# Performance work log

Hardware: AMD Instinct MI355X
Metric: run time of the kernel (lower is better)

The kernel has to match this reference:

```python
import jax, jax.numpy as jnp
import numpy as np

DIM = 256
HEADS = 8
WIN = 8
HIDDEN = 1024
EPS = 1e-5

def _rel_pos_index(w):
    coords = np.stack(np.meshgrid(np.arange(w), np.arange(w), indexing='ij'))  # [2,w,w]
    cf = coords.reshape(2, -1)
    rel = cf[:, :, None] - cf[:, None, :]  # [2,N,N]
    rel = rel.transpose(1, 2, 0)
    rel[:, :, 0] += w - 1
    rel[:, :, 1] += w - 1
    rel[:, :, 0] *= 2 * w - 1
    return jnp.asarray(rel.sum(-1))  # [N,N] int

REL_IDX = _rel_pos_index(WIN)

def _layernorm(x, g, b):
    mu = jnp.mean(x, -1, keepdims=True)
    var = jnp.mean(jnp.square(x - mu), -1, keepdims=True)
    return (x - mu) * jax.lax.rsqrt(var + EPS) * g + b

def setup_inputs() -> dict:
    key = jax.random.key(0)
    ks = jax.random.split(key, 12)
    s = 0.02
    return {
        'x': jax.random.normal(ks[0], (16, 4096, 256), jnp.float32),
        'H': 64,
        'W': 64,
        'ln1_g': jnp.ones((DIM,), jnp.float32),
        'ln1_b': jnp.zeros((DIM,), jnp.float32),
        'qkv_w': jax.random.normal(ks[1], (DIM, 3 * DIM), jnp.float32) * s,
        'proj_w': jax.random.normal(ks[2], (DIM, DIM), jnp.float32) * s,
        'proj_b': jnp.zeros((DIM,), jnp.float32),
        'rel_bias_table': jax.random.normal(ks[3], ((2 * WIN - 1) ** 2, HEADS), jnp.float32) * s,
        'ln2_g': jnp.ones((DIM,), jnp.float32),
        'ln2_b': jnp.zeros((DIM,), jnp.float32),
        'fc1_w': jax.random.normal(ks[4], (DIM, HIDDEN), jnp.float32) * s,
        'fc1_b': jnp.zeros((HIDDEN,), jnp.float32),
        'fc2_w': jax.random.normal(ks[5], (HIDDEN, DIM), jnp.float32) * s,
        'fc2_b': jnp.zeros((DIM,), jnp.float32),
    }

def reference(x, H, W, ln1_g, ln1_b, qkv_w, proj_w, proj_b, rel_bias_table,
              ln2_g, ln2_b, fc1_w, fc1_b, fc2_w, fc2_b):
    B, L, C = x.shape
    w = WIN
    N = w * w
    head_dim = C // HEADS
    scale = head_dim ** -0.5

    shortcut = x
    h = _layernorm(x, ln1_g, ln1_b).reshape(B, H, W, C)
    # H, W chosen divisible by window_size -> pad_h = pad_w = 0 (faithful fast path)
    # window partition: [B*nW, N, C]
    h = h.reshape(B, H // w, w, W // w, w, C).transpose(0, 1, 3, 2, 4, 5)
    xw = h.reshape(-1, N, C)
    Bw = xw.shape[0]

    qkv = (xw @ qkv_w).reshape(Bw, N, 3, HEADS, head_dim)
    q = qkv[:, :, 0].transpose(0, 2, 1, 3) * scale  # [Bw,h,N,d]
    k = qkv[:, :, 1].transpose(0, 2, 1, 3)
    v = qkv[:, :, 2].transpose(0, 2, 1, 3)

    attn = jnp.einsum('bhnd,bhmd->bhnm', q, k)
    bias = rel_bias_table[REL_IDX.reshape(-1)].reshape(N, N, HEADS).transpose(2, 0, 1)
    attn = jax.nn.softmax(attn + bias[None], axis=-1)
    out = jnp.einsum('bhnm,bhmd->bhnd', attn, v).transpose(0, 2, 1, 3).reshape(Bw, N, C)
    out = out @ proj_w + proj_b

    # window reverse
    out = out.reshape(B, H // w, W // w, w, w, C).transpose(0, 1, 3, 2, 4, 5)
    out = out.reshape(B, L, C)

    x = shortcut + out
    h2 = _layernorm(x, ln2_g, ln2_b)
    mlp = jax.nn.gelu(h2 @ fc1_w + fc1_b, approximate=False) @ fc2_w + fc2_b
    return x + mlp
```

## Files before the change

kernel.cpp:

```cpp
#include <hip/hip_runtime.h>
#include <hip/hip_bf16.h>

typedef __attribute__((ext_vector_type(8))) short bf16x8;
typedef __attribute__((ext_vector_type(4))) float f32x4;

typedef __attribute__((address_space(3))) void LdsVoid;
typedef const __attribute__((address_space(1))) void GblVoid;

__device__ __forceinline__ void gload16(const void* g, void* l) {
  __builtin_amdgcn_global_load_lds((GblVoid*)g, (LdsVoid*)l, 16, 0, 0);
}

__device__ __forceinline__ unsigned short f2bf(float f) {
  union { float f; unsigned int u; } x; x.f = f;
  unsigned int r = (x.u + 0x7fffu + ((x.u >> 16) & 1u)) >> 16;
  return (unsigned short)r;
}

__device__ __forceinline__ float gelu_f(float t) {
  float u = t * (0.7978845608028654f + 0.03567740814f * t * t);
  float e = __expf(2.0f * u);
  float th = 1.0f - 2.0f * __builtin_amdgcn_rcpf(e + 1.0f);
  return 0.5f * t * (1.0f + th);
}

__global__ __launch_bounds__(256) void prep_w(
    const float* __restrict__ qw, const float* __restrict__ pw,
    const float* __restrict__ f1, const float* __restrict__ f2,
    unsigned short* __restrict__ out) {
  int idx = blockIdx.x * 256 + threadIdx.x;
  if (idx < 196608) { int n = idx >> 8, k = idx & 255; out[idx] = f2bf(qw[k * 768 + n]); return; }
  int i2 = idx - 196608;
  if (i2 < 65536) { int n = i2 >> 8, k = i2 & 255; out[idx] = f2bf(pw[k * 256 + n]); return; }
  int i3 = i2 - 65536;
  if (i3 < 262144) { int n = i3 >> 8, k = i3 & 255; out[idx] = f2bf(f1[k * 1024 + n]); return; }
  int i4 = i3 - 262144;
  { int n = i4 >> 10, k = i4 & 1023; out[idx] = f2bf(f2[k * 256 + n]); }
}

__global__ __launch_bounds__(256) void ln1_kernel(
    const float* __restrict__ x, const float* __restrict__ g, const float* __restrict__ b,
    unsigned short* __restrict__ xn) {
  int lane = threadIdx.x & 63, wid = threadIdx.x >> 6;
  size_t t = (size_t)blockIdx.x * 4 + wid;
  float4 v = ((const float4*)(x + t * 256))[lane];
  float s = v.x + v.y + v.z + v.w;
  #pragma unroll
  for (int m = 1; m < 64; m <<= 1) s += __shfl_xor(s, m);
  float mean = s * (1.0f / 256.0f);
  float dx = v.x - mean, dy = v.y - mean, dz = v.z - mean, dw = v.w - mean;
  float q = dx * dx + dy * dy + dz * dz + dw * dw;
  #pragma unroll
  for (int m = 1; m < 64; m <<= 1) q += __shfl_xor(q, m);
  float rstd = rsqrtf(q * (1.0f / 256.0f) + 1e-5f);
  float4 gg = ((const float4*)g)[lane];
  float4 bb = ((const float4*)b)[lane];
  unsigned int o0 = f2bf(dx * rstd * gg.x + bb.x) | ((unsigned int)f2bf(dy * rstd * gg.y + bb.y) << 16);
  unsigned int o1 = f2bf(dz * rstd * gg.z + bb.z) | ((unsigned int)f2bf(dw * rstd * gg.w + bb.w) << 16);
  int bI = (int)(t >> 12), rem = (int)t & 4095, y = rem >> 6, xc = rem & 63;
  size_t r = ((size_t)(bI * 64 + (y >> 3) * 8 + (xc >> 3))) * 64 + (y & 7) * 8 + (xc & 7);
  uint2 o; o.x = o0; o.y = o1;
  ((uint2*)(xn + r * 256))[lane] = o;
}

template <int EPI>
__global__ __launch_bounds__(256) void gemm_bt(
    const unsigned short* __restrict__ A, const unsigned short* __restrict__ Bt,
    unsigned short* __restrict__ outb, float* __restrict__ outf,
    const float* __restrict__ bias, const float* __restrict__ xres,
    int M, int N, int K) {
  __shared__ __align__(16) unsigned short lds[2 * 8192];
  const int tid = threadIdx.x;
  const int lane = tid & 63, wid = tid >> 6;
  const int cl = lane & 15, cg = lane >> 4;
  const unsigned nwg = gridDim.x * gridDim.y;
  const unsigned orig = blockIdx.y * gridDim.x + blockIdx.x;
  const unsigned virt = (orig & 7) * (nwg >> 3) + (orig >> 3);
  const unsigned bx = virt % gridDim.x, by = virt / gridDim.x;
  const size_t m0 = (size_t)by * 128;
  const size_t n0 = (size_t)bx * 128;
  const int wr = wid >> 1, wc = wid & 1;
  f32x4 acc[4][4] = {};

  const int r4 = lane >> 2;
  const int gsw = ((lane & 3) ^ ((r4 >> 1) & 3)) * 8;
  const unsigned short* aStage = A + (m0 + wid * 32 + r4) * K + gsw;
  const unsigned short* bStage = Bt + (n0 + wid * 32 + r4) * K + gsw;
  const size_t jstep = (size_t)16 * K;
  const int nt = K >> 5;

  #define STAGE(T, B)                                                   \
    { const int ko_ = (T) * 32;                                         \
      unsigned short* la_ = lds + (B) * 8192 + wid * 1024;              \
      unsigned short* lb_ = la_ + 4096;                                 \
      gload16(aStage + ko_, la_);                                       \
      gload16(aStage + ko_ + jstep, la_ + 512);                         \
      gload16(bStage + ko_, lb_);                                       \
      gload16(bStage + ko_ + jstep, lb_ + 512); }

  bf16x8 af[4], bfr[4];
  const int sl_ = (cg ^ ((cl >> 1) & 3)) * 8;
  #define READF(B)                                                          \
    { const unsigned short* base_ = lds + (B) * 8192;                       \
      _Pragma("unroll")                                                     \
      for (int i = 0; i < 4; ++i) {                                         \
        af[i]  = *(const bf16x8*)(base_ + (wr * 64 + i * 16 + cl) * 32 + sl_);        \
        bfr[i] = *(const bf16x8*)(base_ + 4096 + (wc * 64 + i * 16 + cl) * 32 + sl_); \
      } }

  #define MFMAS()                                                           \
    { _Pragma("unroll")                                                     \
      for (int mi = 0; mi < 4; ++mi)                                        \
        _Pragma("unroll")                                                   \
        for (int ni = 0; ni < 4; ++ni)                                      \
          acc[mi][ni] = __builtin_amdgcn_mfma_f32_16x16x32_bf16(bfr[ni], af[mi], acc[mi][ni], 0, 0, 0); }

  STAGE(0, 0);
  STAGE(1, 1);
  for (int t = 0; t < nt; ++t) {
    if (t == nt - 1) { asm volatile("s_waitcnt vmcnt(0)" ::: "memory"); }
    else             { asm volatile("s_waitcnt vmcnt(4)" ::: "memory"); }
    __builtin_amdgcn_s_barrier();
    READF(t & 1);
    __builtin_amdgcn_sched_barrier(0);
    asm volatile("s_waitcnt lgkmcnt(0)" ::: "memory");
    __builtin_amdgcn_s_barrier();
    __builtin_amdgcn_sched_barrier(0);
    if (t + 2 < nt) STAGE(t + 2, t & 1);
    MFMAS();
  }
  #undef STAGE
  #undef READF
  #undef MFMAS

  #pragma unroll
  for (int mi = 0; mi < 4; ++mi) {
    const size_t row = m0 + wr * 64 + mi * 16 + cl;
    #pragma unroll
    for (int ni = 0; ni < 4; ++ni) {
      const size_t col = n0 + wc * 64 + ni * 16 + cg * 4;
      f32x4 v = acc[mi][ni];
      if (EPI == 0) {
        uint2 o;
        o.x = f2bf(v[0]) | ((unsigned int)f2bf(v[1]) << 16);
        o.y = f2bf(v[2]) | ((unsigned int)f2bf(v[3]) << 16);
        *(uint2*)&outb[row * N + col] = o;
      } else if (EPI == 1) {
        float4 bb = *(const float4*)&bias[col];
        float g0 = gelu_f(v[0] + bb.x), g1 = gelu_f(v[1] + bb.y);
        float g2 = gelu_f(v[2] + bb.z), g3 = gelu_f(v[3] + bb.w);
        uint2 o;
        o.x = f2bf(g0) | ((unsigned int)f2bf(g1) << 16);
        o.y = f2bf(g2) | ((unsigned int)f2bf(g3) << 16);
        *(uint2*)&outb[row * N + col] = o;
      } else if (EPI == 3) {
        float4 bb = *(const float4*)&bias[col];
        float4* p = (float4*)&outf[row * N + col];
        float4 old = *p;
        old.x += v[0] + bb.x; old.y += v[1] + bb.y;
        old.z += v[2] + bb.z; old.w += v[3] + bb.w;
        *p = old;
      } else if (EPI == 4) {
        int winr = (int)(row >> 6), pos = (int)(row & 63);
        int bI = winr >> 6, wy = (winr >> 3) & 7, wx = winr & 7;
        size_t tt = (size_t)bI * 4096 + (size_t)(wy * 8 + (pos >> 3)) * 64 + wx * 8 + (pos & 7);
        float4 bb = *(const float4*)&bias[col];
        float4 xr = *(const float4*)&xres[tt * 256 + col];
        float4 o;
        o.x = v[0] + bb.x + xr.x; o.y = v[1] + bb.y + xr.y;
        o.z = v[2] + bb.z + xr.z; o.w = v[3] + bb.w + xr.w;
        *(float4*)&outf[tt * 256 + col] = o;
      }
    }
  }
}

__global__ __launch_bounds__(256) void attn_win(
    const unsigned short* __restrict__ qkv, const float* __restrict__ table,
    unsigned short* __restrict__ out) {
  __shared__ float tbl[1800];
  __shared__ __align__(16) unsigned short p_lds[4][64 * 72];
  __shared__ __align__(16) unsigned short vt_lds[4][32 * 72];
  const int tid = threadIdx.x, lane = tid & 63, wid = tid >> 6;
  const int cl = lane & 15, cg = lane >> 4;
  for (int i = tid; i < 1800; i += 256) tbl[i] = table[i];
  __syncthreads();
  const size_t wbase = (size_t)blockIdx.x * 64;
  unsigned short* P = p_lds[wid];
  unsigned short* VT = vt_lds[wid];
  const float scale = 0.17677669529663687f;

  for (int hh = 0; hh < 2; ++hh) {
    const int h = wid + hh * 4;
    const int qoff = h * 32, koff = 256 + h * 32, voff = 512 + h * 32;
    bf16x8 qf[4], kf[4];
    #pragma unroll
    for (int mi = 0; mi < 4; ++mi)
      qf[mi] = *(const bf16x8*)&qkv[(wbase + mi * 16 + cl) * 768 + qoff + cg * 8];
    #pragma unroll
    for (int nj = 0; nj < 4; ++nj)
      kf[nj] = *(const bf16x8*)&qkv[(wbase + nj * 16 + cl) * 768 + koff + cg * 8];
    f32x4 S[4][4] = {};
    #pragma unroll
    for (int mi = 0; mi < 4; ++mi)
      #pragma unroll
      for (int nj = 0; nj < 4; ++nj)
        S[mi][nj] = __builtin_amdgcn_mfma_f32_16x16x32_bf16(qf[mi], kf[nj], S[mi][nj], 0, 0, 0);

    {
      const unsigned short* vrow = &qkv[(wbase + lane) * 768 + voff];
      unsigned short tmp[32];
      #pragma unroll
      for (int p = 0; p < 4; ++p) *(uint4*)&tmp[p * 8] = ((const uint4*)vrow)[p];
      #pragma unroll
      for (int d = 0; d < 32; ++d) VT[d * 72 + lane] = tmp[d];
    }

    #pragma unroll
    for (int mi = 0; mi < 4; ++mi) {
      #pragma unroll
      for (int r = 0; r < 4; ++r) {
        const int i = mi * 16 + cg * 4 + r;
        const int yi = i >> 3, xi = i & 7;
        float v[4];
        float m = -1e30f;
        #pragma unroll
        for (int nj = 0; nj < 4; ++nj) {
          const int j = nj * 16 + cl;
          const int yj = j >> 3, xj = j & 7;
          float bia = tbl[((yi - yj + 7) * 15 + (xi - xj + 7)) * 8 + h];
          v[nj] = S[mi][nj][r] * scale + bia;
          m = fmaxf(m, v[nj]);
        }
        #pragma unroll
        for (int mk = 1; mk < 16; mk <<= 1) m = fmaxf(m, __shfl_xor(m, mk));
        float s = 0.0f;
        #pragma unroll
        for (int nj = 0; nj < 4; ++nj) { v[nj] = __expf(v[nj] - m); s += v[nj]; }
        #pragma unroll
        for (int mk = 1; mk < 16; mk <<= 1) s += __shfl_xor(s, mk);
        const float rinv = __builtin_amdgcn_rcpf(s);
        #pragma unroll
        for (int nj = 0; nj < 4; ++nj) P[i * 72 + nj * 16 + cl] = f2bf(v[nj] * rinv);
      }
    }

    f32x4 O[4][2] = {};
    #pragma unroll
    for (int ks = 0; ks < 2; ++ks) {
      bf16x8 pa[4], vb[2];
      #pragma unroll
      for (int mi = 0; mi < 4; ++mi)
        pa[mi] = *(const bf16x8*)&P[(mi * 16 + cl) * 72 + ks * 32 + cg * 8];
      #pragma unroll
      for (int nd = 0; nd < 2; ++nd)
        vb[nd] = *(const bf16x8*)&VT[(nd * 16 + cl) * 72 + ks * 32 + cg * 8];
      #pragma unroll
      for (int mi = 0; mi < 4; ++mi)
        #pragma unroll
        for (int nd = 0; nd < 2; ++nd)
          O[mi][nd] = __builtin_amdgcn_mfma_f32_16x16x32_bf16(vb[nd], pa[mi], O[mi][nd], 0, 0, 0);
    }

    #pragma unroll
    for (int mi = 0; mi < 4; ++mi)
      #pragma unroll
      for (int nd = 0; nd < 2; ++nd) {
        uint2 o;
        o.x = f2bf(O[mi][nd][0]) | ((unsigned int)f2bf(O[mi][nd][1]) << 16);
        o.y = f2bf(O[mi][nd][2]) | ((unsigned int)f2bf(O[mi][nd][3]) << 16);
        *(uint2*)&out[(wbase + mi * 16 + cl) * 256 + h * 32 + nd * 16 + cg * 4] = o;
      }
  }
}

__global__ __launch_bounds__(256) void ln2_kernel(
    const float* __restrict__ x2, const float* __restrict__ g, const float* __restrict__ b,
    unsigned short* __restrict__ h2) {
  int lane = threadIdx.x & 63, wid = threadIdx.x >> 6;
  size_t t = (size_t)blockIdx.x * 4 + wid;
  float4 v = ((const float4*)(x2 + t * 256))[lane];
  float s = v.x + v.y + v.z + v.w;
  #pragma unroll
  for (int m = 1; m < 64; m <<= 1) s += __shfl_xor(s, m);
  float mean = s * (1.0f / 256.0f);
  float dx = v.x - mean, dy = v.y - mean, dz = v.z - mean, dw = v.w - mean;
  float q = dx * dx + dy * dy + dz * dz + dw * dw;
  #pragma unroll
  for (int m = 1; m < 64; m <<= 1) q += __shfl_xor(q, m);
  float rstd = rsqrtf(q * (1.0f / 256.0f) + 1e-5f);
  float4 gg = ((const float4*)g)[lane];
  float4 bb = ((const float4*)b)[lane];
  uint2 o;
  o.x = f2bf(dx * rstd * gg.x + bb.x) | ((unsigned int)f2bf(dy * rstd * gg.y + bb.y) << 16);
  o.y = f2bf(dz * rstd * gg.z + bb.z) | ((unsigned int)f2bf(dw * rstd * gg.w + bb.w) << 16);
  ((uint2*)(h2 + t * 256))[lane] = o;
}

extern "C" void kernel_launch(void* const* d_in, const int* in_sizes, int n_in,
                              void* d_out, int out_size, void* d_ws, size_t ws_size,
                              hipStream_t stream) {
  (void)in_sizes; (void)n_in; (void)out_size; (void)ws_size;
  const float* x       = (const float*)d_in[0];
  const float* ln1_g   = (const float*)d_in[3];
  const float* ln1_b   = (const float*)d_in[4];
  const float* qkv_w   = (const float*)d_in[5];
  const float* proj_w  = (const float*)d_in[6];
  const float* proj_b  = (const float*)d_in[7];
  const float* rel_tbl = (const float*)d_in[8];
  const float* ln2_g   = (const float*)d_in[9];
  const float* ln2_b   = (const float*)d_in[10];
  const float* fc1_w   = (const float*)d_in[11];
  const float* fc1_b   = (const float*)d_in[12];
  const float* fc2_w   = (const float*)d_in[13];
  const float* fc2_b   = (const float*)d_in[14];
  float* out = (float*)d_out;

  char* ws = (char*)d_ws;
  const size_t OFF_XN   = 1572864;
  const size_t OFF_QKV  = OFF_XN + 33554432;
  const size_t OFF_ATTN = OFF_QKV + 100663296;
  unsigned short* Wt      = (unsigned short*)ws;
  unsigned short* xn      = (unsigned short*)(ws + OFF_XN);
  unsigned short* h2      = xn;
  unsigned short* qkv     = (unsigned short*)(ws + OFF_QKV);
  unsigned short* fc1out  = (unsigned short*)(ws + OFF_QKV);
  unsigned short* attnout = (unsigned short*)(ws + OFF_ATTN);

  prep_w<<<3072, 256, 0, stream>>>(qkv_w, proj_w, fc1_w, fc2_w, Wt);
  ln1_kernel<<<16384, 256, 0, stream>>>(x, ln1_g, ln1_b, xn);
  gemm_bt<0><<<dim3(6, 512), 256, 0, stream>>>(xn, Wt, qkv, nullptr, nullptr, nullptr, 65536, 768, 256);
  attn_win<<<1024, 256, 0, stream>>>(qkv, rel_tbl, attnout);
  gemm_bt<4><<<dim3(2, 512), 256, 0, stream>>>(attnout, Wt + 196608, nullptr, out, proj_b, x, 65536, 256, 256);
  ln2_kernel<<<16384, 256, 0, stream>>>(out, ln2_g, ln2_b, h2);
  gemm_bt<1><<<dim3(8, 512), 256, 0, stream>>>(h2, Wt + 262144, fc1out, nullptr, fc1_b, nullptr, 65536, 1024, 256);
  gemm_bt<3><<<dim3(2, 512), 256, 0, stream>>>(fc1out, Wt + 524288, nullptr, out, fc2_b, nullptr, 65536, 256, 1024);
}
```

Before: 430.6 us.

## Replace 128x128 GEMM with 256x256 8-wave ping-pong pipelined GEMM

Replaces the 4-wave 128x128-tile GEMM with an 8-wave kernel that computes 256x256 tiles using a 64-wide K step, 128 KB of dynamic LDS, and a four-phase loop. Each phase issues LDS reads and global-to-LDS loads for quarter-tiles and runs MFMA under raised priority. The goal is more operand reuse per loaded byte and better overlap of memory traffic with MFMA work. The larger tile halves or thirds the grid sizes, which lowers parallelism across the 65536-row GEMMs. With 128 KB of LDS per block, occupancy is probably about one block per CU, which may not match launch_bounds(512,2), and the extra barriers add synchronisation cost.

```diff
diff --git a/kernel.cpp b/kernel.cpp
--- a/kernel.cpp
+++ b/kernel.cpp
@@ -64,82 +64,113 @@
 }
 
 template <int EPI>
-__global__ __launch_bounds__(256) void gemm_bt(
+__global__ __launch_bounds__(512, 2) void gemm8p(
     const unsigned short* __restrict__ A, const unsigned short* __restrict__ Bt,
     unsigned short* __restrict__ outb, float* __restrict__ outf,
     const float* __restrict__ bias, const float* __restrict__ xres,
     int M, int N, int K) {
-  __shared__ __align__(16) unsigned short lds[2 * 8192];
+  extern __shared__ unsigned short lds[];
   const int tid = threadIdx.x;
-  const int lane = tid & 63, wid = tid >> 6;
+  const int lane = tid & 63, w = tid >> 6;
   const int cl = lane & 15, cg = lane >> 4;
+  const int wr = w >> 2, wc = w & 3;
   const unsigned nwg = gridDim.x * gridDim.y;
   const unsigned orig = blockIdx.y * gridDim.x + blockIdx.x;
   const unsigned virt = (orig & 7) * (nwg >> 3) + (orig >> 3);
   const unsigned bx = virt % gridDim.x, by = virt / gridDim.x;
-  const size_t m0 = (size_t)by * 128;
-  const size_t n0 = (size_t)bx * 128;
-  const int wr = wid >> 1, wc = wid & 1;
-  f32x4 acc[4][4] = {};
-
-  const int r4 = lane >> 2;
-  const int gsw = ((lane & 3) ^ ((r4 >> 1) & 3)) * 8;
-  const unsigned short* aStage = A + (m0 + wid * 32 + r4) * K + gsw;
-  const unsigned short* bStage = Bt + (n0 + wid * 32 + r4) * K + gsw;
-  const size_t jstep = (size_t)16 * K;
-  const int nt = K >> 5;
-
-  #define STAGE(T, B)                                                   \
-    { const int ko_ = (T) * 32;                                         \
-      unsigned short* la_ = lds + (B) * 8192 + wid * 1024;              \
-      unsigned short* lb_ = la_ + 4096;                                 \
-      gload16(aStage + ko_, la_);                                       \
-      gload16(aStage + ko_ + jstep, la_ + 512);                         \
-      gload16(bStage + ko_, lb_);                                       \
-      gload16(bStage + ko_ + jstep, lb_ + 512); }
-
-  bf16x8 af[4], bfr[4];
-  const int sl_ = (cg ^ ((cl >> 1) & 3)) * 8;
-  #define READF(B)                                                          \
-    { const unsigned short* base_ = lds + (B) * 8192;                       \
-      _Pragma("unroll")                                                     \
-      for (int i = 0; i < 4; ++i) {                                         \
-        af[i]  = *(const bf16x8*)(base_ + (wr * 64 + i * 16 + cl) * 32 + sl_);        \
-        bfr[i] = *(const bf16x8*)(base_ + 4096 + (wc * 64 + i * 16 + cl) * 32 + sl_); \
-      } }
-
-  #define MFMAS()                                                           \
-    { _Pragma("unroll")                                                     \
-      for (int mi = 0; mi < 4; ++mi)                                        \
-        _Pragma("unroll")                                                   \
-        for (int ni = 0; ni < 4; ++ni)                                      \
-          acc[mi][ni] = __builtin_amdgcn_mfma_f32_16x16x32_bf16(bfr[ni], af[mi], acc[mi][ni], 0, 0, 0); }
-
-  STAGE(0, 0);
-  STAGE(1, 1);
-  for (int t = 0; t < nt; ++t) {
-    if (t == nt - 1) { asm volatile("s_waitcnt vmcnt(0)" ::: "memory"); }
-    else             { asm volatile("s_waitcnt vmcnt(4)" ::: "memory"); }
-    __builtin_amdgcn_s_barrier();
-    READF(t & 1);
-    __builtin_amdgcn_sched_barrier(0);
-    asm volatile("s_waitcnt lgkmcnt(0)" ::: "memory");
-    __builtin_amdgcn_s_barrier();
-    __builtin_amdgcn_sched_barrier(0);
-    if (t + 2 < nt) STAGE(t + 2, t & 1);
-    MFMAS();
+  const size_t m0 = (size_t)by * 256, n0 = (size_t)bx * 256;
+  const int nkt = K >> 6;
+
+  const int trow = tid >> 3, tslot = tid & 7;
+  const unsigned short* aSrc = A + (m0 + trow) * K + (tslot ^ (trow & 7)) * 8;
+  const unsigned short* bSrc = Bt + (n0 + trow) * K + (tslot ^ (trow & 7)) * 8;
+
+  const int slk0 = ((0 + cg) ^ (cl & 7)) * 8;
+  const int slk1 = ((4 + cg) ^ (cl & 7)) * 8;
+
+  f32x4 acc[8][4] = {};
+  bf16x8 af[2][4], b0[2][2], b1[2][2];
+
+  #define STAGE(ISB, KT, HALF)                                                    \
+    { unsigned short* d_ = lds + (ISB) * 32768 + ((KT) & 1) * 16384 +             \
+                           (HALF) * 8192 + tid * 8;                               \
+      const unsigned short* s_ = ((ISB) ? bSrc : aSrc) +                          \
+                                 (size_t)((HALF) * 128) * K + (KT) * 64;          \
+      gload16(s_, d_); gload16(s_ + (size_t)64 * K, d_ + 4096); }
+
+  #define READ_A(MH, P)                                                           \
+    { const unsigned short* ba_ = lds + (P) * 16384 + (MH) * 8192 +               \
+                                  (wr * 64 + cl) * 64;                            \
+      _Pragma("unroll")                                                           \
+      for (int mi = 0; mi < 4; ++mi) {                                            \
+        af[0][mi] = *(const bf16x8*)(ba_ + mi * 1024 + slk0);                     \
+        af[1][mi] = *(const bf16x8*)(ba_ + mi * 1024 + slk1); } }
+
+  #define READ_B(NH, P, D)                                                        \
+    { const unsigned short* bb_ = lds + 32768 + (P) * 16384 + (NH) * 8192 +       \
+                                  (wc * 32 + cl) * 64;                            \
+      _Pragma("unroll")                                                           \
+      for (int ni = 0; ni < 2; ++ni) {                                            \
+        D[0][ni] = *(const bf16x8*)(bb_ + ni * 1024 + slk0);                      \
+        D[1][ni] = *(const bf16x8*)(bb_ + ni * 1024 + slk1); } }
+
+  #define MFMA_Q(MH, NH, D)                                                       \
+    { _Pragma("unroll")                                                           \
+      for (int kk = 0; kk < 2; ++kk)                                              \
+        _Pragma("unroll")                                                         \
+        for (int mi = 0; mi < 4; ++mi)                                            \
+          _Pragma("unroll")                                                       \
+          for (int ni = 0; ni < 2; ++ni)                                          \
+            acc[(MH) * 4 + mi][(NH) * 2 + ni] =                                   \
+                __builtin_amdgcn_mfma_f32_16x16x32_bf16(                          \
+                    D[kk][ni], af[kk][mi], acc[(MH) * 4 + mi][(NH) * 2 + ni],     \
+                    0, 0, 0); }
+
+  #define BAR() __builtin_amdgcn_s_barrier()
+  #define LGKM0() { asm volatile("s_waitcnt lgkmcnt(0)" ::: "memory");            \
+                    __builtin_amdgcn_sched_barrier(0); }
+
+  STAGE(0, 0, 0); STAGE(1, 0, 1); STAGE(1, 0, 0); STAGE(0, 0, 1);
+  STAGE(0, 1, 0); STAGE(1, 1, 1);
+  asm volatile("s_waitcnt vmcnt(4)" ::: "memory");
+  BAR();
+
+  for (int kt = 0; kt < nkt; ++kt) {
+    const int p = kt & 1;
+    READ_A(0, p); READ_B(0, p, b0);
+    if (kt + 1 < nkt) STAGE(1, kt + 1, 0);
+    BAR(); LGKM0();
+    __builtin_amdgcn_s_setprio(1); MFMA_Q(0, 0, b0); __builtin_amdgcn_s_setprio(0);
+    BAR();
+    READ_B(1, p, b1);
+    if (kt + 1 < nkt) STAGE(0, kt + 1, 1);
+    BAR(); LGKM0();
+    __builtin_amdgcn_s_setprio(1); MFMA_Q(0, 1, b1); __builtin_amdgcn_s_setprio(0);
+    BAR();
+    READ_A(1, p);
+    if (kt + 2 < nkt) STAGE(0, kt + 2, 0);
+    BAR(); LGKM0();
+    __builtin_amdgcn_s_setprio(1); MFMA_Q(1, 1, b1); __builtin_amdgcn_s_setprio(0);
+    BAR();
+    if (kt + 2 < nkt) STAGE(1, kt + 2, 1);
+    BAR();
+    __builtin_amdgcn_s_setprio(1); MFMA_Q(1, 0, b0); __builtin_amdgcn_s_setprio(0);
+    if (kt + 2 < nkt) { asm volatile("s_waitcnt vmcnt(4)" ::: "memory"); }
+    else              { asm volatile("s_waitcnt vmcnt(0)" ::: "memory"); }
+    BAR();
   }
   #undef STAGE
-  #undef READF
-  #undef MFMAS
-
-  #pragma unroll
-  for (int mi = 0; mi < 4; ++mi) {
-    const size_t row = m0 + wr * 64 + mi * 16 + cl;
-    #pragma unroll
-    for (int ni = 0; ni < 4; ++ni) {
-      const size_t col = n0 + wc * 64 + ni * 16 + cg * 4;
-      f32x4 v = acc[mi][ni];
+  #undef READ_A
+  #undef READ_B
+  #undef MFMA_Q
+
+  #pragma unroll
+  for (int mi8 = 0; mi8 < 8; ++mi8) {
+    const size_t row = m0 + (mi8 >> 2) * 128 + wr * 64 + (mi8 & 3) * 16 + cl;
+    #pragma unroll
+    for (int ni4 = 0; ni4 < 4; ++ni4) {
+      const size_t col = n0 + (ni4 >> 1) * 128 + wc * 32 + (ni4 & 1) * 16 + cg * 4;
+      f32x4 v = acc[mi8][ni4];
       if (EPI == 0) {
         uint2 o;
         o.x = f2bf(v[0]) | ((unsigned int)f2bf(v[1]) << 16);
@@ -155,11 +186,11 @@
         *(uint2*)&outb[row * N + col] = o;
       } else if (EPI == 3) {
         float4 bb = *(const float4*)&bias[col];
-        float4* p = (float4*)&outf[row * N + col];
-        float4 old = *p;
+        float4* pp = (float4*)&outf[row * N + col];
+        float4 old = *pp;
         old.x += v[0] + bb.x; old.y += v[1] + bb.y;
         old.z += v[2] + bb.z; old.w += v[3] + bb.w;
-        *p = old;
+        *pp = old;
       } else if (EPI == 4) {
         int winr = (int)(row >> 6), pos = (int)(row & 63);
         int bI = winr >> 6, wy = (winr >> 3) & 7, wx = winr & 7;
@@ -327,12 +358,19 @@
   unsigned short* fc1out  = (unsigned short*)(ws + OFF_QKV);
   unsigned short* attnout = (unsigned short*)(ws + OFF_ATTN);
 
+  static int attr_done = -1;
+  if (attr_done < 0) attr_done = 0;
+  hipFuncSetAttribute((const void*)gemm8p<0>, hipFuncAttributeMaxDynamicSharedMemorySize, 131072);
+  hipFuncSetAttribute((const void*)gemm8p<1>, hipFuncAttributeMaxDynamicSharedMemorySize, 131072);
+  hipFuncSetAttribute((const void*)gemm8p<3>, hipFuncAttributeMaxDynamicSharedMemorySize, 131072);
+  hipFuncSetAttribute((const void*)gemm8p<4>, hipFuncAttributeMaxDynamicSharedMemorySize, 131072);
+
   prep_w<<<3072, 256, 0, stream>>>(qkv_w, proj_w, fc1_w, fc2_w, Wt);
   ln1_kernel<<<16384, 256, 0, stream>>>(x, ln1_g, ln1_b, xn);
-  gemm_bt<0><<<dim3(6, 512), 256, 0, stream>>>(xn, Wt, qkv, nullptr, nullptr, nullptr, 65536, 768, 256);
+  gemm8p<0><<<dim3(3, 256), 512, 131072, stream>>>(xn, Wt, qkv, nullptr, nullptr, nullptr, 65536, 768, 256);
   attn_win<<<1024, 256, 0, stream>>>(qkv, rel_tbl, attnout);
-  gemm_bt<4><<<dim3(2, 512), 256, 0, stream>>>(attnout, Wt + 196608, nullptr, out, proj_b, x, 65536, 256, 256);
+  gemm8p<4><<<dim3(1, 256), 512, 131072, stream>>>(attnout, Wt + 196608, nullptr, out, proj_b, x, 65536, 256, 256);
   ln2_kernel<<<16384, 256, 0, stream>>>(out, ln2_g, ln2_b, h2);
-  gemm_bt<1><<<dim3(8, 512), 256, 0, stream>>>(h2, Wt + 262144, fc1out, nullptr, fc1_b, nullptr, 65536, 1024, 256);
-  gemm_bt<3><<<dim3(2, 512), 256, 0, stream>>>(fc1out, Wt + 524288, nullptr, out, fc2_b, nullptr, 65536, 256, 1024);
-}
+  gemm8p<1><<<dim3(4, 256), 512, 131072, stream>>>(h2, Wt + 262144, fc1out, nullptr, fc1_b, nullptr, 65536, 1024, 256);
+  gemm8p<3><<<dim3(1, 256), 512, 131072, stream>>>(fc1out, Wt + 524288, nullptr, out, fc2_b, nullptr, 65536, 256, 1024);
+}
```

Result: no change. 424.3 us (-1.4%).

## Replace LDS-staged GEMM with register-resident weight tiles and direct A loads

Applied to the files above, without the earlier changes.

The shared-memory double-buffered GEMM is replaced by a kernel that keeps a 64-column slice of the weight matrix, for a full 256-wide K chunk, in registers. Each wave streams its A rows straight from global memory with one-step register prefetch and covers 128 rows in two 64-row tiles. This removes LDS staging, barriers and waitcnt handling, and reuses the loaded weights across both row tiles when K fits in one chunk. The costs are high register pressure (32 bf16x8 weight fragments per lane), uncoalesced 16-byte A loads with no cross-wave sharing, and each A row being reloaded once per 64-column block, which can make the kernel bandwidth-bound.

```diff
diff --git a/kernel.cpp b/kernel.cpp
--- a/kernel.cpp
+++ b/kernel.cpp
@@ -3,13 +3,6 @@
 
 typedef __attribute__((ext_vector_type(8))) short bf16x8;
 typedef __attribute__((ext_vector_type(4))) float f32x4;
-
-typedef __attribute__((address_space(3))) void LdsVoid;
-typedef const __attribute__((address_space(1))) void GblVoid;
-
-__device__ __forceinline__ void gload16(const void* g, void* l) {
-  __builtin_amdgcn_global_load_lds((GblVoid*)g, (LdsVoid*)l, 16, 0, 0);
-}
 
 __device__ __forceinline__ unsigned short f2bf(float f) {
   union { float f; unsigned int u; } x; x.f = f;
@@ -63,113 +56,97 @@
   ((uint2*)(xn + r * 256))[lane] = o;
 }
 
-template <int EPI>
-__global__ __launch_bounds__(256) void gemm_bt(
+template <int EPI, int KC>
+__global__ __launch_bounds__(256, 2) void gemm_flat(
     const unsigned short* __restrict__ A, const unsigned short* __restrict__ Bt,
     unsigned short* __restrict__ outb, float* __restrict__ outf,
     const float* __restrict__ bias, const float* __restrict__ xres,
-    int M, int N, int K) {
-  __shared__ __align__(16) unsigned short lds[2 * 8192];
-  const int tid = threadIdx.x;
-  const int lane = tid & 63, wid = tid >> 6;
+    int N, int K) {
+  const int tid = threadIdx.x, lane = tid & 63, w = tid >> 6;
   const int cl = lane & 15, cg = lane >> 4;
-  const unsigned nwg = gridDim.x * gridDim.y;
-  const unsigned orig = blockIdx.y * gridDim.x + blockIdx.x;
-  const unsigned virt = (orig & 7) * (nwg >> 3) + (orig >> 3);
-  const unsigned bx = virt % gridDim.x, by = virt / gridDim.x;
-  const size_t m0 = (size_t)by * 128;
-  const size_t n0 = (size_t)bx * 128;
-  const int wr = wid >> 1, wc = wid & 1;
-  f32x4 acc[4][4] = {};
-
-  const int r4 = lane >> 2;
-  const int gsw = ((lane & 3) ^ ((r4 >> 1) & 3)) * 8;
-  const unsigned short* aStage = A + (m0 + wid * 32 + r4) * K + gsw;
-  const unsigned short* bStage = Bt + (n0 + wid * 32 + r4) * K + gsw;
-  const size_t jstep = (size_t)16 * K;
-  const int nt = K >> 5;
-
-  #define STAGE(T, B)                                                   \
-    { const int ko_ = (T) * 32;                                         \
-      unsigned short* la_ = lds + (B) * 8192 + wid * 1024;              \
-      unsigned short* lb_ = la_ + 4096;                                 \
-      gload16(aStage + ko_, la_);                                       \
-      gload16(aStage + ko_ + jstep, la_ + 512);                         \
-      gload16(bStage + ko_, lb_);                                       \
-      gload16(bStage + ko_ + jstep, lb_ + 512); }
-
-  bf16x8 af[4], bfr[4];
-  const int sl_ = (cg ^ ((cl >> 1) & 3)) * 8;
-  #define READF(B)                                                          \
-    { const unsigned short* base_ = lds + (B) * 8192;                       \
-      _Pragma("unroll")                                                     \
-      for (int i = 0; i < 4; ++i) {                                         \
-        af[i]  = *(const bf16x8*)(base_ + (wr * 64 + i * 16 + cl) * 32 + sl_);        \
-        bfr[i] = *(const bf16x8*)(base_ + 4096 + (wc * 64 + i * 16 + cl) * 32 + sl_); \
-      } }
-
-  #define MFMAS()                                                           \
-    { _Pragma("unroll")                                                     \
-      for (int mi = 0; mi < 4; ++mi)                                        \
-        _Pragma("unroll")                                                   \
-        for (int ni = 0; ni < 4; ++ni)                                      \
-          acc[mi][ni] = __builtin_amdgcn_mfma_f32_16x16x32_bf16(bfr[ni], af[mi], acc[mi][ni], 0, 0, 0); }
-
-  STAGE(0, 0);
-  STAGE(1, 1);
-  for (int t = 0; t < nt; ++t) {
-    if (t == nt - 1) { asm volatile("s_waitcnt vmcnt(0)" ::: "memory"); }
-    else             { asm volatile("s_waitcnt vmcnt(4)" ::: "memory"); }
-    __builtin_amdgcn_s_barrier();
-    READF(t & 1);
-    __builtin_amdgcn_sched_barrier(0);
-    asm volatile("s_waitcnt lgkmcnt(0)" ::: "memory");
-    __builtin_amdgcn_s_barrier();
-    __builtin_amdgcn_sched_barrier(0);
-    if (t + 2 < nt) STAGE(t + 2, t & 1);
-    MFMAS();
-  }
-  #undef STAGE
-  #undef READF
-  #undef MFMAS
-
-  #pragma unroll
-  for (int mi = 0; mi < 4; ++mi) {
-    const size_t row = m0 + wr * 64 + mi * 16 + cl;
-    #pragma unroll
-    for (int ni = 0; ni < 4; ++ni) {
-      const size_t col = n0 + wc * 64 + ni * 16 + cg * 4;
-      f32x4 v = acc[mi][ni];
-      if (EPI == 0) {
-        uint2 o;
-        o.x = f2bf(v[0]) | ((unsigned int)f2bf(v[1]) << 16);
-        o.y = f2bf(v[2]) | ((unsigned int)f2bf(v[3]) << 16);
-        *(uint2*)&outb[row * N + col] = o;
-      } else if (EPI == 1) {
-        float4 bb = *(const float4*)&bias[col];
-        float g0 = gelu_f(v[0] + bb.x), g1 = gelu_f(v[1] + bb.y);
-        float g2 = gelu_f(v[2] + bb.z), g3 = gelu_f(v[3] + bb.w);
-        uint2 o;
-        o.x = f2bf(g0) | ((unsigned int)f2bf(g1) << 16);
-        o.y = f2bf(g2) | ((unsigned int)f2bf(g3) << 16);
-        *(uint2*)&outb[row * N + col] = o;
-      } else if (EPI == 3) {
-        float4 bb = *(const float4*)&bias[col];
-        float4* p = (float4*)&outf[row * N + col];
-        float4 old = *p;
-        old.x += v[0] + bb.x; old.y += v[1] + bb.y;
-        old.z += v[2] + bb.z; old.w += v[3] + bb.w;
-        *p = old;
-      } else if (EPI == 4) {
-        int winr = (int)(row >> 6), pos = (int)(row & 63);
-        int bI = winr >> 6, wy = (winr >> 3) & 7, wx = winr & 7;
-        size_t tt = (size_t)bI * 4096 + (size_t)(wy * 8 + (pos >> 3)) * 64 + wx * 8 + (pos & 7);
-        float4 bb = *(const float4*)&bias[col];
-        float4 xr = *(const float4*)&xres[tt * 256 + col];
-        float4 o;
-        o.x = v[0] + bb.x + xr.x; o.y = v[1] + bb.y + xr.y;
-        o.z = v[2] + bb.z + xr.z; o.w = v[3] + bb.w + xr.w;
-        *(float4*)&outf[tt * 256 + col] = o;
+  const int n0 = blockIdx.x * 64;
+  const size_t K_ = (size_t)K;
+  const size_t mWave = (size_t)blockIdx.y * 512 + (size_t)w * 128;
+
+  bf16x8 wf[4][8];
+
+  #pragma unroll
+  for (int i = 0; i < 2; ++i) {
+    f32x4 acc[4][4] = {};
+    const size_t mTile = mWave + (size_t)i * 64;
+    const unsigned short* aBase = A + (mTile + cl) * K_ + cg * 8;
+
+    #pragma unroll
+    for (int kc = 0; kc < KC; ++kc) {
+      const int kOff = kc * 256;
+      if (KC != 1 || i == 0) {
+        #pragma unroll
+        for (int t = 0; t < 4; ++t)
+          #pragma unroll
+          for (int kt = 0; kt < 8; ++kt)
+            wf[t][kt] = *(const bf16x8*)&Bt[(size_t)(n0 + t * 16 + cl) * K_ + kOff + kt * 32 + cg * 8];
+      }
+      bf16x8 acur[4], anxt[4];
+      #pragma unroll
+      for (int mi = 0; mi < 4; ++mi)
+        acur[mi] = *(const bf16x8*)&aBase[(size_t)mi * 16 * K_ + kOff];
+      #pragma unroll
+      for (int kt = 0; kt < 8; ++kt) {
+        if (kt < 7) {
+          #pragma unroll
+          for (int mi = 0; mi < 4; ++mi)
+            anxt[mi] = *(const bf16x8*)&aBase[(size_t)mi * 16 * K_ + kOff + (kt + 1) * 32];
+        }
+        #pragma unroll
+        for (int mi = 0; mi < 4; ++mi)
+          #pragma unroll
+          for (int ni = 0; ni < 4; ++ni)
+            acc[mi][ni] = __builtin_amdgcn_mfma_f32_16x16x32_bf16(wf[ni][kt], acur[mi], acc[mi][ni], 0, 0, 0);
+        if (kt < 7) {
+          #pragma unroll
+          for (int mi = 0; mi < 4; ++mi) acur[mi] = anxt[mi];
+        }
+      }
+    }
+
+    #pragma unroll
+    for (int mi = 0; mi < 4; ++mi) {
+      const size_t row = mTile + mi * 16 + cl;
+      #pragma unroll
+      for (int ni = 0; ni < 4; ++ni) {
+        const size_t col = n0 + ni * 16 + cg * 4;
+        f32x4 v = acc[mi][ni];
+        if (EPI == 0) {
+          uint2 o;
+          o.x = f2bf(v[0]) | ((unsigned int)f2bf(v[1]) << 16);
+          o.y = f2bf(v[2]) | ((unsigned int)f2bf(v[3]) << 16);
+          *(uint2*)&outb[row * N + col] = o;
+        } else if (EPI == 1) {
+          float4 bb = *(const float4*)&bias[col];
+          float g0 = gelu_f(v[0] + bb.x), g1 = gelu_f(v[1] + bb.y);
+          float g2 = gelu_f(v[2] + bb.z), g3 = gelu_f(v[3] + bb.w);
+          uint2 o;
+          o.x = f2bf(g0) | ((unsigned int)f2bf(g1) << 16);
+          o.y = f2bf(g2) | ((unsigned int)f2bf(g3) << 16);
+          *(uint2*)&outb[row * N + col] = o;
+        } else if (EPI == 3) {
+          float4 bb = *(const float4*)&bias[col];
+          float4* pp = (float4*)&outf[row * N + col];
+          float4 old = *pp;
+          old.x += v[0] + bb.x; old.y += v[1] + bb.y;
+          old.z += v[2] + bb.z; old.w += v[3] + bb.w;
+          *pp = old;
+        } else if (EPI == 4) {
+          int winr = (int)(row >> 6), pos = (int)(row & 63);
+          int bI = winr >> 6, wy = (winr >> 3) & 7, wx = winr & 7;
+          size_t tt = (size_t)bI * 4096 + (size_t)(wy * 8 + (pos >> 3)) * 64 + wx * 8 + (pos & 7);
+          float4 bb = *(const float4*)&bias[col];
+          float4 xr = *(const float4*)&xres[tt * 256 + col];
+          float4 o;
+          o.x = v[0] + bb.x + xr.x; o.y = v[1] + bb.y + xr.y;
+          o.z = v[2] + bb.z + xr.z; o.w = v[3] + bb.w + xr.w;
+          *(float4*)&outf[tt * 256 + col] = o;
+        }
       }
     }
   }
@@ -329,10 +306,10 @@
 
   prep_w<<<3072, 256, 0, stream>>>(qkv_w, proj_w, fc1_w, fc2_w, Wt);
   ln1_kernel<<<16384, 256, 0, stream>>>(x, ln1_g, ln1_b, xn);
-  gemm_bt<0><<<dim3(6, 512), 256, 0, stream>>>(xn, Wt, qkv, nullptr, nullptr, nullptr, 65536, 768, 256);
+  gemm_flat<0, 1><<<dim3(12, 128), 256, 0, stream>>>(xn, Wt, qkv, nullptr, nullptr, nullptr, 768, 256);
   attn_win<<<1024, 256, 0, stream>>>(qkv, rel_tbl, attnout);
-  gemm_bt<4><<<dim3(2, 512), 256, 0, stream>>>(attnout, Wt + 196608, nullptr, out, proj_b, x, 65536, 256, 256);
+  gemm_flat<4, 1><<<dim3(4, 128), 256, 0, stream>>>(attnout, Wt + 196608, nullptr, out, proj_b, x, 256, 256);
   ln2_kernel<<<16384, 256, 0, stream>>>(out, ln2_g, ln2_b, h2);
-  gemm_bt<1><<<dim3(8, 512), 256, 0, stream>>>(h2, Wt + 262144, fc1out, nullptr, fc1_b, nullptr, 65536, 1024, 256);
-  gemm_bt<3><<<dim3(2, 512), 256, 0, stream>>>(fc1out, Wt + 524288, nullptr, out, fc2_b, nullptr, 65536, 256, 1024);
-}
+  gemm_flat<1, 1><<<dim3(16, 128), 256, 0, stream>>>(h2, Wt + 262144, fc1out, nullptr, fc1_b, nullptr, 1024, 256);
+  gemm_flat<3, 4><<<dim3(4, 128), 256, 0, stream>>>(fc1out, Wt + 524288, nullptr, out, fc2_b, nullptr, 256, 1024);
+}
```

After: 727.3 us. 68.9% more time.
